# Kernel optimization log

Hardware: AMD Instinct MI355X
Metric: run time of the kernel (lower is better)

Reference implementation:

```python
import jax, jax.numpy as jnp
import numpy as np

B, T, D, H, F = 4, 2048, 1024, 16, 4096
HD = D // H
EPS = 1e-5


def setup_inputs() -> dict:
    key = jax.random.key(0)
    ks = jax.random.split(key, 10)
    s = lambda fan_in: 1.0 / np.sqrt(fan_in)
    return {
        "x": jax.random.normal(ks[0], (B, T, D), jnp.float32),
        "ln1_g": jnp.ones((D,), jnp.float32),
        "ln1_b": jnp.zeros((D,), jnp.float32),
        "ln2_g": jnp.ones((D,), jnp.float32),
        "ln2_b": jnp.zeros((D,), jnp.float32),
        "Wq": jax.random.normal(ks[1], (H, D, HD), jnp.float32) * s(D),
        "Wk": jax.random.normal(ks[2], (H, D, HD), jnp.float32) * s(D),
        "Wv": jax.random.normal(ks[3], (H, D, HD), jnp.float32) * s(D),
        "Wo": jax.random.normal(ks[4], (D, D), jnp.float32) * s(D),
        "bo": jnp.zeros((D,), jnp.float32),
        "W1": jax.random.normal(ks[5], (D, F), jnp.float32) * s(D),
        "b1": jnp.zeros((F,), jnp.float32),
        "W2": jax.random.normal(ks[6], (F, D), jnp.float32) * s(F),
        "b2": jnp.zeros((D,), jnp.float32),
    }


def _layernorm(x, g, b):
    mu = jnp.mean(x, axis=-1, keepdims=True)
    var = jnp.mean(jnp.square(x - mu), axis=-1, keepdims=True)
    return (x - mu) * jax.lax.rsqrt(var + EPS) * g + b


def reference(x, ln1_g, ln1_b, ln2_g, ln2_b, Wq, Wk, Wv, Wo, bo, W1, b1, W2, b2):
    Bc, Tc, Dc = x.shape
    xn = _layernorm(x, ln1_g, ln1_b)
    # per-head projections (source loops over heads; here batched over h)
    q = jnp.einsum('btd,hdk->bhtk', xn, Wq)
    k = jnp.einsum('btd,hdk->bhtk', xn, Wk)
    v = jnp.einsum('btd,hdk->bhtk', xn, Wv)
    scale = jnp.asarray(Dc, x.dtype) ** -0.5  # C**-0.5 with C = embedding_dim
    scores = jnp.einsum('bhtk,bhsk->bhts', q, k) * scale
    causal = jnp.tril(jnp.ones((Tc, Tc), bool))
    scores = jnp.where(causal, scores, -jnp.inf)
    attn = jax.nn.softmax(scores, axis=-1)
    out = jnp.einsum('bhts,bhsk->bhtk', attn, v)
    out = out.transpose(0, 2, 1, 3).reshape(Bc, Tc, Dc)  # concat heads
    attn_out = out @ Wo + bo
    h = attn_out + x  # residual 1
    hn = _layernorm(h, ln2_g, ln2_b)
    ff = jax.nn.relu(hn @ W1 + b1) @ W2 + b2
    return ff + h  # residual 2
```

## Files before the change

### kernel.cpp

```cpp
#include <hip/hip_runtime.h>
#include <hip/hip_bf16.h>

#define NB 4
#define NT 2048
#define ND 1024
#define NH 16
#define NHD 64
#define NF 4096
#define MTOK (NB*NT)

typedef float f32x4 __attribute__((ext_vector_type(4)));
typedef __bf16 bf16x8 __attribute__((ext_vector_type(8)));
typedef short s16x8 __attribute__((ext_vector_type(8)));
typedef unsigned short ushort_t;

__device__ inline ushort_t f2bf(float f) {
    unsigned int u = __builtin_bit_cast(unsigned int, f);
    unsigned int r = (u + 0x7FFFu + ((u >> 16) & 1u)) >> 16;
    return (ushort_t)r;
}
__device__ inline float bf2f(ushort_t u) {
    return __builtin_bit_cast(float, (unsigned int)u << 16);
}

__device__ __forceinline__ void async_load16(const void* g, void* l) {
    __builtin_amdgcn_global_load_lds(
        (const __attribute__((address_space(1))) void*)g,
        (__attribute__((address_space(3))) void*)l, 16, 0, 0);
}

__device__ __forceinline__ unsigned int cvt_pk_bf16(float lo, float hi) {
    unsigned int r;
    asm("v_cvt_pk_bf16_f32 %0, %1, %2" : "=v"(r) : "v"(lo), "v"(hi));
    return r;
}

__device__ __forceinline__ float exp2_fast(float x) {
    float r;
    asm("v_exp_f32 %0, %1" : "=v"(r) : "v"(x));
    return r;
}

__global__ __launch_bounds__(256)
void transpose_to_bf16(const float* __restrict__ src, ushort_t* __restrict__ dst,
                       int R, int C) {
    __shared__ float tile[32][33];
    int c0 = blockIdx.x * 32, r0 = blockIdx.y * 32;
    #pragma unroll
    for (int i = 0; i < 32; i += 8)
        tile[threadIdx.y + i][threadIdx.x] =
            src[(size_t)(r0 + threadIdx.y + i) * C + c0 + threadIdx.x];
    __syncthreads();
    #pragma unroll
    for (int i = 0; i < 32; i += 8)
        dst[(size_t)(c0 + threadIdx.y + i) * R + r0 + threadIdx.x] =
            f2bf(tile[threadIdx.x][threadIdx.y + i]);
}

__global__ __launch_bounds__(256)
void transpose_qkv_to_bf16(const float* __restrict__ Wq, const float* __restrict__ Wk,
                           const float* __restrict__ Wv, ushort_t* __restrict__ dst) {
    __shared__ float tile[32][33];
    int z = blockIdx.z;
    int w = z >> 4, h = z & 15;
    const float* src = (w == 0 ? Wq : (w == 1 ? Wk : Wv)) + (size_t)h * ND * NHD;
    const float sc = (w == 0) ? 0.03125f * 1.44269504f : 1.0f;
    ushort_t* out = dst + ((size_t)w * ND + h * NHD) * ND;
    int c0 = blockIdx.x * 32, r0 = blockIdx.y * 32;
    #pragma unroll
    for (int i = 0; i < 32; i += 8)
        tile[threadIdx.y + i][threadIdx.x] =
            src[(size_t)(r0 + threadIdx.y + i) * NHD + c0 + threadIdx.x];
    __syncthreads();
    #pragma unroll
    for (int i = 0; i < 32; i += 8)
        out[(size_t)(c0 + threadIdx.y + i) * ND + r0 + threadIdx.x] =
            f2bf(tile[threadIdx.x][threadIdx.y + i] * sc);
}

__global__ __launch_bounds__(256)
void layernorm_to_bf16(const float* __restrict__ x, const float* __restrict__ g,
                       const float* __restrict__ bvec, ushort_t* __restrict__ out) {
    int row = blockIdx.x;
    const float4* xr = (const float4*)(x + (size_t)row * ND);
    float4 v = xr[threadIdx.x];
    float s = v.x + v.y + v.z + v.w;
    float s2 = v.x * v.x + v.y * v.y + v.z * v.z + v.w * v.w;
    #pragma unroll
    for (int o = 32; o >= 1; o >>= 1) {
        s += __shfl_xor(s, o);
        s2 += __shfl_xor(s2, o);
    }
    __shared__ float red[8];
    int wave = threadIdx.x >> 6, lane = threadIdx.x & 63;
    if (lane == 0) { red[wave] = s; red[4 + wave] = s2; }
    __syncthreads();
    float ts = red[0] + red[1] + red[2] + red[3];
    float ts2 = red[4] + red[5] + red[6] + red[7];
    float mu = ts * (1.f / ND);
    float var = ts2 * (1.f / ND) - mu * mu;
    float rs = rsqrtf(var + 1e-5f);
    float4 gv = ((const float4*)g)[threadIdx.x];
    float4 bv = ((const float4*)bvec)[threadIdx.x];
    ushort4 o4;
    o4.x = f2bf((v.x - mu) * rs * gv.x + bv.x);
    o4.y = f2bf((v.y - mu) * rs * gv.y + bv.y);
    o4.z = f2bf((v.z - mu) * rs * gv.z + bv.z);
    o4.w = f2bf((v.w - mu) * rs * gv.w + bv.w);
    ((ushort4*)(out + (size_t)row * ND))[threadIdx.x] = o4;
}

__global__ __launch_bounds__(256)
void layernorm_bf16(const ushort_t* __restrict__ x, const float* __restrict__ g,
                    const float* __restrict__ bvec, ushort_t* __restrict__ out) {
    int row = blockIdx.x;
    ushort4 u4 = ((const ushort4*)(x + (size_t)row * ND))[threadIdx.x];
    float4 v;
    v.x = bf2f(u4.x); v.y = bf2f(u4.y); v.z = bf2f(u4.z); v.w = bf2f(u4.w);
    float s = v.x + v.y + v.z + v.w;
    float s2 = v.x * v.x + v.y * v.y + v.z * v.z + v.w * v.w;
    #pragma unroll
    for (int o = 32; o >= 1; o >>= 1) {
        s += __shfl_xor(s, o);
        s2 += __shfl_xor(s2, o);
    }
    __shared__ float red[8];
    int wave = threadIdx.x >> 6, lane = threadIdx.x & 63;
    if (lane == 0) { red[wave] = s; red[4 + wave] = s2; }
    __syncthreads();
    float ts = red[0] + red[1] + red[2] + red[3];
    float ts2 = red[4] + red[5] + red[6] + red[7];
    float mu = ts * (1.f / ND);
    float var = ts2 * (1.f / ND) - mu * mu;
    float rs = rsqrtf(var + 1e-5f);
    float4 gv = ((const float4*)g)[threadIdx.x];
    float4 bv = ((const float4*)bvec)[threadIdx.x];
    ushort4 o4;
    o4.x = f2bf((v.x - mu) * rs * gv.x + bv.x);
    o4.y = f2bf((v.y - mu) * rs * gv.y + bv.y);
    o4.z = f2bf((v.z - mu) * rs * gv.z + bv.z);
    o4.w = f2bf((v.w - mu) * rs * gv.w + bv.w);
    ((ushort4*)(out + (size_t)row * ND))[threadIdx.x] = o4;
}

template<int BN, bool HAS_BIAS, bool RELU, int RES_MODE, bool OUT_F32, int OUT_MODE = 0>
__global__ __launch_bounds__(512, 2)
void gemm8p(const ushort_t* __restrict__ A, const ushort_t* __restrict__ Bt,
            const float* __restrict__ bias, const void* __restrict__ res,
            void* __restrict__ outp, ushort_t* __restrict__ vTp,
            int M, int N, int K) {
    constexpr int NFR = BN / 64;
    __shared__ __align__(16) ushort_t As[2][256 * 64];
    __shared__ __align__(16) ushort_t Bs[2][BN * 64];
    const int t = threadIdx.x;
    const int wave = t >> 6, lane = t & 63;
    const int wm = wave >> 2, wn = wave & 3;
    const int g = lane >> 4, l16 = lane & 15;
    int wid = blockIdx.y * gridDim.x + blockIdx.x;
    const int cpx = (gridDim.x * gridDim.y) >> 3;
    wid = (wid & 7) * cpx + (wid >> 3);
    const int m0 = (wid / gridDim.x) * 256;
    const int n0 = (wid % gridDim.x) * BN;
    const int lrow8 = lane >> 3;
    const int srcCol = ((lane & 7) ^ lrow8) * 8;
    const ushort_t* Abase = A + (size_t)m0 * K + srcCol;
    const ushort_t* Bbase = Bt + (size_t)n0 * K + srcCol;
    const int NKT = K >> 6;

    f32x4 acc[8][NFR] = {};

    auto stageAhalf = [&](int kt, int h, int slot) {
        #pragma unroll
        for (int j = 2 * h; j < 2 * h + 2; j++) {
            const int rowbase = j * 64 + wave * 8;
            async_load16(Abase + (size_t)(rowbase + lrow8) * K + kt * 64,
                         &As[slot][rowbase * 64]);
        }
    };
    auto stageBhalf = [&](int kt, int h, int slot) {
        if constexpr (BN == 256) {
            #pragma unroll
            for (int j = 2 * h; j < 2 * h + 2; j++) {
                const int rowbase = j * 64 + wave * 8;
                async_load16(Bbase + (size_t)(rowbase + lrow8) * K + kt * 64,
                             &Bs[slot][rowbase * 64]);
            }
        } else {
            const int rowbase = h * 64 + wave * 8;
            async_load16(Bbase + (size_t)(rowbase + lrow8) * K + kt * 64,
                         &Bs[slot][rowbase * 64]);
        }
    };

    stageAhalf(0, 0, 0); stageAhalf(0, 1, 0);
    stageBhalf(0, 0, 0); stageBhalf(0, 1, 0);
    stageBhalf(1, 0, 1); stageBhalf(1, 1, 1);
    stageAhalf(1, 0, 1);
    if constexpr (BN == 256) asm volatile("s_waitcnt vmcnt(6)" ::: "memory");
    else                     asm volatile("s_waitcnt vmcnt(4)" ::: "memory");
    __builtin_amdgcn_s_barrier();
    __builtin_amdgcn_sched_barrier(0);

    for (int kt = 0; kt < NKT; ++kt) {
        const int cur = kt & 1, nxt = cur ^ 1;
        const ushort_t* as = As[cur];
        const ushort_t* bs = Bs[cur];
        bf16x8 bfr[NFR][2];

        if constexpr (BN == 128) {
            #pragma unroll
            for (int ph = 0; ph < 2; ph++) {
                if (ph == 0) {
                    #pragma unroll
                    for (int nf = 0; nf < NFR; nf++)
                        #pragma unroll
                        for (int ks = 0; ks < 2; ks++) {
                            const int row = wn * (BN / 4) + nf * 16 + l16;
                            int a = row * 128 + ks * 64 + 16 * g;
                            a ^= (row & 7) << 4;
                            bfr[nf][ks] = *(const bf16x8*)((const char*)bs + a);
                        }
                }
                bf16x8 af[2][2][2];
                #pragma unroll
                for (int qq = 0; qq < 2; qq++)
                    #pragma unroll
                    for (int mi2 = 0; mi2 < 2; mi2++)
                        #pragma unroll
                        for (int ks = 0; ks < 2; ks++) {
                            const int row = (ph * 2 + qq) * 64 + wm * 32 + mi2 * 16 + l16;
                            int a = row * 128 + ks * 64 + 16 * g;
                            a ^= (row & 7) << 4;
                            af[qq][mi2][ks] = *(const bf16x8*)((const char*)as + a);
                        }
                if (ph == 0) {
                    if (kt + 1 < NKT) stageAhalf(kt + 1, 1, nxt);
                } else {
                    if (kt + 2 < NKT) {
                        stageBhalf(kt + 2, 0, cur);
                        stageBhalf(kt + 2, 1, cur);
                        stageAhalf(kt + 2, 0, cur);
                    }
                }
                __builtin_amdgcn_sched_barrier(0);
                if (ph == 1) {
                    if (kt >= NKT - 2) asm volatile("s_waitcnt vmcnt(0)" ::: "memory");
                    else               asm volatile("s_waitcnt vmcnt(4)" ::: "memory");
                }
                __builtin_amdgcn_s_barrier();
                __builtin_amdgcn_sched_barrier(0);
                __builtin_amdgcn_s_setprio(1);
                #pragma unroll
                for (int qq = 0; qq < 2; qq++)
                    #pragma unroll
                    for (int mi2 = 0; mi2 < 2; mi2++)
                        #pragma unroll
                        for (int nf = 0; nf < NFR; nf++)
                            #pragma unroll
                            for (int ks = 0; ks < 2; ks++)
                                acc[(ph * 2 + qq) * 2 + mi2][nf] =
                                    __builtin_amdgcn_mfma_f32_16x16x32_bf16(
                                        af[qq][mi2][ks], bfr[nf][ks],
                                        acc[(ph * 2 + qq) * 2 + mi2][nf], 0, 0, 0);
                __builtin_amdgcn_s_setprio(0);
                __builtin_amdgcn_s_barrier();
                __builtin_amdgcn_sched_barrier(0);
            }
        } else {
            #pragma unroll
            for (int q = 0; q < 4; q++) {
                if (q == 0) {
                    #pragma unroll
                    for (int nf = 0; nf < NFR; nf++)
                        #pragma unroll
                        for (int ks = 0; ks < 2; ks++) {
                            const int row = wn * (BN / 4) + nf * 16 + l16;
                            int a = row * 128 + ks * 64 + 16 * g;
                            a ^= (row & 7) << 4;
                            bfr[nf][ks] = *(const bf16x8*)((const char*)bs + a);
                        }
                }
                bf16x8 af[2][2];
                #pragma unroll
                for (int mi2 = 0; mi2 < 2; mi2++)
                    #pragma unroll
                    for (int ks = 0; ks < 2; ks++) {
                        const int row = q * 64 + wm * 32 + mi2 * 16 + l16;
                        int a = row * 128 + ks * 64 + 16 * g;
                        a ^= (row & 7) << 4;
                        af[mi2][ks] = *(const bf16x8*)((const char*)as + a);
                    }
                if (q == 0)      { if (kt + 1 < NKT) stageAhalf(kt + 1, 1, nxt); }
                else if (q == 1) { if (kt + 2 < NKT) stageBhalf(kt + 2, 0, cur); }
                else if (q == 2) { if (kt + 2 < NKT) stageBhalf(kt + 2, 1, cur); }
                else             { if (kt + 2 < NKT) stageAhalf(kt + 2, 0, cur); }
                __builtin_amdgcn_sched_barrier(0);
                if (q == 3) {
                    if (kt >= NKT - 2) asm volatile("s_waitcnt vmcnt(0)" ::: "memory");
                    else               asm volatile("s_waitcnt vmcnt(6)" ::: "memory");
                }
                __builtin_amdgcn_s_barrier();
                __builtin_amdgcn_sched_barrier(0);
                __builtin_amdgcn_s_setprio(1);
                #pragma unroll
                for (int mi2 = 0; mi2 < 2; mi2++)
                    #pragma unroll
                    for (int nf = 0; nf < NFR; nf++)
                        #pragma unroll
                        for (int ks = 0; ks < 2; ks++)
                            acc[q * 2 + mi2][nf] = __builtin_amdgcn_mfma_f32_16x16x32_bf16(
                                af[mi2][ks], bfr[nf][ks], acc[q * 2 + mi2][nf], 0, 0, 0);
                __builtin_amdgcn_s_setprio(0);
                __builtin_amdgcn_s_barrier();
                __builtin_amdgcn_sched_barrier(0);
            }
        }
    }

    const int gc0 = n0 + wn * (BN / 4) + l16;
    if constexpr (OUT_MODE == 1) {
        if (n0 >= 2048) {
            #pragma unroll
            for (int mi = 0; mi < 8; mi++) {
                const int rowb = m0 + (mi >> 1) * 64 + wm * 32 + (mi & 1) * 16 + g * 4;
                const int b = rowb >> 11, tt = rowb & 2047;
                #pragma unroll
                for (int nf = 0; nf < NFR; nf++) {
                    const int col = gc0 + nf * 16;
                    ushort4 o4;
                    o4.x = f2bf(acc[mi][nf][0]);
                    o4.y = f2bf(acc[mi][nf][1]);
                    o4.z = f2bf(acc[mi][nf][2]);
                    o4.w = f2bf(acc[mi][nf][3]);
                    *(ushort4*)(vTp + (size_t)(b * 1024 + col - 2048) * NT + tt) = o4;
                }
            }
            return;
        }
    }
    #pragma unroll
    for (int mi = 0; mi < 8; mi++) {
        const int rowb = m0 + (mi >> 1) * 64 + wm * 32 + (mi & 1) * 16 + g * 4;
        #pragma unroll
        for (int nf = 0; nf < NFR; nf++) {
            const int col = gc0 + nf * 16;
            float bb = 0.f;
            if constexpr (HAS_BIAS) bb = bias[col];
            #pragma unroll
            for (int r = 0; r < 4; r++) {
                const int row = rowb + r;
                float v = acc[mi][nf][r] + bb;
                if constexpr (RELU) v = fmaxf(v, 0.f);
                if constexpr (RES_MODE == 1)
                    v += ((const float*)res)[(size_t)row * N + col];
                else if constexpr (RES_MODE == 2)
                    v += bf2f(((const ushort_t*)res)[(size_t)row * N + col]);
                if constexpr (OUT_F32)
                    ((float*)outp)[(size_t)row * N + col] = v;
                else
                    ((ushort_t*)outp)[(size_t)row * N + col] = f2bf(v);
            }
        }
    }
}

template<bool HAS_BIAS, bool RELU, int RES_MODE, bool OUT_F32>
__global__ __launch_bounds__(256, 2)
void gemm2b64(const ushort_t* __restrict__ A, const ushort_t* __restrict__ Bt,
              const float* __restrict__ bias, const void* __restrict__ res,
              void* __restrict__ outp, int M, int N, int K) {
    __shared__ __align__(16) ushort_t As[2][128 * 64];
    __shared__ __align__(16) ushort_t Bs[2][128 * 64];
    const int t = threadIdx.x;
    const int wave = t >> 6, lane = t & 63;
    const int wm = wave >> 1, wn = wave & 1;
    const int g = lane >> 4, l16 = lane & 15;
    int wid = blockIdx.y * gridDim.x + blockIdx.x;
    const int cpx = (gridDim.x * gridDim.y) >> 3;
    wid = (wid & 7) * cpx + (wid >> 3);
    const int m0 = (wid / gridDim.x) * 128;
    const int n0 = (wid % gridDim.x) * 128;
    const int rw = lane >> 3, ck = lane & 7;
    const int srcCol = (ck ^ rw) * 8;
    const ushort_t* Abase = A + (size_t)m0 * K + srcCol;
    const ushort_t* Bbase = Bt + (size_t)n0 * K + srcCol;
    const int NKT = K >> 6;

    f32x4 acc[4][4] = {};

    auto stage = [&](int kt, int slot) {
        #pragma unroll
        for (int j = 0; j < 4; j++) {
            const int rowbase = j * 32 + wave * 8;
            async_load16(Abase + (size_t)(rowbase + rw) * K + kt * 64,
                         &As[slot][rowbase * 64]);
        }
        #pragma unroll
        for (int j = 0; j < 4; j++) {
            const int rowbase = j * 32 + wave * 8;
            async_load16(Bbase + (size_t)(rowbase + rw) * K + kt * 64,
                         &Bs[slot][rowbase * 64]);
        }
    };

    stage(0, 0);
    stage(1, 1);

    for (int kt = 0; kt < NKT; ++kt) {
        const int cur = kt & 1;
        if (kt >= NKT - 1) asm volatile("s_waitcnt vmcnt(0)" ::: "memory");
        else               asm volatile("s_waitcnt vmcnt(8)" ::: "memory");
        __builtin_amdgcn_s_barrier();
        __builtin_amdgcn_sched_barrier(0);

        const ushort_t* as = As[cur];
        const ushort_t* bs = Bs[cur];
        bf16x8 af[4][2], bfr[4][2];
        #pragma unroll
        for (int mi = 0; mi < 4; mi++)
            #pragma unroll
            for (int ks = 0; ks < 2; ks++) {
                const int row = wm * 64 + mi * 16 + l16;
                int a = row * 128 + ks * 64 + 16 * g;
                a ^= (row & 7) << 4;
                af[mi][ks] = *(const bf16x8*)((const char*)as + a);
            }
        #pragma unroll
        for (int nf = 0; nf < 4; nf++)
            #pragma unroll
            for (int ks = 0; ks < 2; ks++) {
                const int row = wn * 64 + nf * 16 + l16;
                int a = row * 128 + ks * 64 + 16 * g;
                a ^= (row & 7) << 4;
                bfr[nf][ks] = *(const bf16x8*)((const char*)bs + a);
            }
        __builtin_amdgcn_s_setprio(1);
        #pragma unroll
        for (int mi = 0; mi < 4; mi++)
            #pragma unroll
            for (int nf = 0; nf < 4; nf++)
                #pragma unroll
                for (int ks = 0; ks < 2; ks++)
                    acc[mi][nf] = __builtin_amdgcn_mfma_f32_16x16x32_bf16(
                        af[mi][ks], bfr[nf][ks], acc[mi][nf], 0, 0, 0);
        __builtin_amdgcn_s_setprio(0);
        __builtin_amdgcn_s_barrier();
        __builtin_amdgcn_sched_barrier(0);
        if (kt + 2 < NKT) stage(kt + 2, cur);
    }

    const int gc0 = n0 + wn * 64 + l16;
    #pragma unroll
    for (int mi = 0; mi < 4; mi++) {
        const int rowb = m0 + wm * 64 + mi * 16 + g * 4;
        #pragma unroll
        for (int nf = 0; nf < 4; nf++) {
            const int col = gc0 + nf * 16;
            float bb = 0.f;
            if constexpr (HAS_BIAS) bb = bias[col];
            #pragma unroll
            for (int r = 0; r < 4; r++) {
                const int row = rowb + r;
                float v = acc[mi][nf][r] + bb;
                if constexpr (RELU) v = fmaxf(v, 0.f);
                if constexpr (RES_MODE == 1)
                    v += ((const float*)res)[(size_t)row * N + col];
                else if constexpr (RES_MODE == 2)
                    v += bf2f(((const ushort_t*)res)[(size_t)row * N + col]);
                if constexpr (OUT_F32)
                    ((float*)outp)[(size_t)row * N + col] = v;
                else
                    ((ushort_t*)outp)[(size_t)row * N + col] = f2bf(v);
            }
        }
    }
}

__global__ __launch_bounds__(256)
void attn_kernel(const ushort_t* __restrict__ qkv, const ushort_t* __restrict__ vT,
                 ushort_t* __restrict__ out) {
    __shared__ __align__(16) ushort_t Ks[2][64 * 64];
    __shared__ __align__(16) ushort_t Vt[2][64 * 64];
    __shared__ unsigned int Pw[4][32][35];
    const int L = blockIdx.y * gridDim.x + blockIdx.x;
    const int xcd = L & 7, kk = L >> 3;
    const int bh = ((kk & 7) << 3) | xcd;
    const int pairIdx = kk >> 3;
    const int b = bh >> 4, h = bh & 15;
    const int t = threadIdx.x, wave = t >> 6, lane = t & 63;
    const int g = lane >> 4, q16 = lane & 15;
    const size_t base = ((size_t)b * NT) * 3072 + h * NHD;
    const ushort_t* qp_base = qkv + base;
    const ushort_t* kb = qkv + base + 1024;
    const ushort_t* vbt = vT + (size_t)bh * 64 * NT;
    const int krw = lane >> 3, kck = lane & 7;
    const int ksrc = (kck ^ krw) * 8;

    bf16x8 ones_f;
    {
        uint4 u = {0x3F803F80u, 0x3F803F80u, 0x3F803F80u, 0x3F803F80u};
        ones_f = __builtin_bit_cast(bf16x8, u);
    }

    auto stageK = [&](int kv, int buf) {
        #pragma unroll
        for (int c = 0; c < 2; c++) {
            const int rowbase = c * 32 + wave * 8;
            async_load16(kb + (size_t)(kv * 64 + rowbase + krw) * 3072 + ksrc,
                         &Ks[buf][rowbase * 64]);
        }
    };
    auto stageV = [&](int kv, int buf) {
        #pragma unroll
        for (int c = 0; c < 2; c++) {
            const int rowbase = c * 32 + wave * 8;
            const int scol = ((kck ^ krw ^ ((c * 4 + wave) & 7)) * 8);
            async_load16(vbt + (size_t)(rowbase + krw) * NT + kv * 64 + scol,
                         &Vt[buf][rowbase * 64]);
        }
    };

    for (int half = 0; half < 2; half++) {
        const int qt = half ? (15 - pairIdx) : pairIdx;
        const int q0 = qt * 128;
        const int wq0 = q0 + wave * 32;
        bf16x8 qf[2][2];
        #pragma unroll
        for (int qb2 = 0; qb2 < 2; qb2++) {
            const ushort_t* qp = qp_base + (size_t)(wq0 + 16 * qb2 + q16) * 3072 + 8 * g;
            qf[qb2][0] = *(const bf16x8*)qp;
            qf[qb2][1] = *(const bf16x8*)(qp + 32);
        }
        f32x4 of[2][4] = {};
        f32x4 of4[2] = {};
        const int nkv = 2 * qt + 2;

        stageK(0, 0);
        stageV(0, 0);
        __syncthreads();

        for (int kv = 0; kv < nkv; ++kv) {
            const int cur = kv & 1, nxt = cur ^ 1;
            if (kv + 1 < nkv) {
                stageK(kv + 1, nxt);
                stageV(kv + 1, nxt);
            }
            __builtin_amdgcn_sched_barrier(0);

            const int kbase = kv * 64;
            if (kbase <= wq0 + 31) {
                bf16x8 kf[4][2];
                #pragma unroll
                for (int n = 0; n < 4; n++)
                    #pragma unroll
                    for (int kd = 0; kd < 2; kd++) {
                        int row = n * 16 + q16;
                        int a = row * 128 + (kd * 64 + 16 * g);
                        a ^= ((row & 7) << 4);
                        kf[n][kd] = *(const bf16x8*)((const char*)&Ks[cur][0] + a);
                    }

                f32x4 sf[2][4] = {};
                #pragma unroll
                for (int n = 0; n < 4; n++)
                    #pragma unroll
                    for (int kd = 0; kd < 2; kd++) {
                        sf[0][n] = __builtin_amdgcn_mfma_f32_16x16x32_bf16(
                            kf[n][kd], qf[0][kd], sf[0][n], 0, 0, 0);
                        sf[1][n] = __builtin_amdgcn_mfma_f32_16x16x32_bf16(
                            kf[n][kd], qf[1][kd], sf[1][n], 0, 0, 0);
                    }

                #pragma unroll
                for (int qb2 = 0; qb2 < 2; qb2++) {
                    const int wqb = wq0 + 16 * qb2 + q16;
                    const bool partial = (kbase + 63 > wq0 + 16 * qb2);
                    float p[4][4];
                    #pragma unroll
                    for (int n = 0; n < 4; n++)
                        #pragma unroll
                        for (int r = 0; r < 4; r++) {
                            float v = sf[qb2][n][r];
                            if (partial) {
                                int kg = kbase + n * 16 + 4 * g + r;
                                if (kg > wqb) v = -1.0e30f;
                            }
                            p[n][r] = exp2_fast(v);
                        }
                    unsigned int* pr = &Pw[wave][16 * qb2 + q16][0];
                    #pragma unroll
                    for (int n = 0; n < 4; n++) {
                        pr[8 * n + 2 * g + 0] = cvt_pk_bf16(p[n][0], p[n][1]);
                        pr[8 * n + 2 * g + 1] = cvt_pk_bf16(p[n][2], p[n][3]);
                    }
                }

                #pragma unroll
                for (int kbk = 0; kbk < 2; kbk++) {
                    bf16x8 pfr[2];
                    #pragma unroll
                    for (int qb2 = 0; qb2 < 2; qb2++) {
                        const unsigned int* pr = &Pw[wave][16 * qb2 + q16][0];
                        uint4 pu;
                        pu.x = pr[16 * kbk + 4 * g + 0];
                        pu.y = pr[16 * kbk + 4 * g + 1];
                        pu.z = pr[16 * kbk + 4 * g + 2];
                        pu.w = pr[16 * kbk + 4 * g + 3];
                        pfr[qb2] = __builtin_bit_cast(bf16x8, pu);
                    }
                    of4[0] = __builtin_amdgcn_mfma_f32_16x16x32_bf16(
                        ones_f, pfr[0], of4[0], 0, 0, 0);
                    of4[1] = __builtin_amdgcn_mfma_f32_16x16x32_bf16(
                        ones_f, pfr[1], of4[1], 0, 0, 0);
                    #pragma unroll
                    for (int nf = 0; nf < 4; nf++) {
                        const int d = nf * 16 + q16;
                        int a = (d << 7) + (kbk * 64 + 16 * g);
                        a ^= (((d & 7) ^ ((d >> 3) & 7)) << 4);
                        bf16x8 vf = *(const bf16x8*)((const char*)&Vt[cur][0] + a);
                        of[0][nf] = __builtin_amdgcn_mfma_f32_16x16x32_bf16(
                            vf, pfr[0], of[0][nf], 0, 0, 0);
                        of[1][nf] = __builtin_amdgcn_mfma_f32_16x16x32_bf16(
                            vf, pfr[1], of[1][nf], 0, 0, 0);
                    }
                }
            }

            __syncthreads();
        }

        #pragma unroll
        for (int qb2 = 0; qb2 < 2; qb2++) {
            float rl = 1.f / of4[qb2][0];
            const size_t orow = (size_t)b * NT + q0 + wave * 32 + 16 * qb2 + q16;
            #pragma unroll
            for (int nf = 0; nf < 4; nf++) {
                ushort4 o4;
                o4.x = f2bf(of[qb2][nf][0] * rl);
                o4.y = f2bf(of[qb2][nf][1] * rl);
                o4.z = f2bf(of[qb2][nf][2] * rl);
                o4.w = f2bf(of[qb2][nf][3] * rl);
                *(ushort4*)(out + orow * ND + h * NHD + nf * 16 + 4 * g) = o4;
            }
        }
    }
}

extern "C" void kernel_launch(void* const* d_in, const int* in_sizes, int n_in,
                              void* d_out, int out_size, void* d_ws, size_t ws_size,
                              hipStream_t stream) {
    const float* x     = (const float*)d_in[0];
    const float* ln1_g = (const float*)d_in[1];
    const float* ln1_b = (const float*)d_in[2];
    const float* ln2_g = (const float*)d_in[3];
    const float* ln2_b = (const float*)d_in[4];
    const float* Wq    = (const float*)d_in[5];
    const float* Wk    = (const float*)d_in[6];
    const float* Wv    = (const float*)d_in[7];
    const float* Wo    = (const float*)d_in[8];
    const float* bo    = (const float*)d_in[9];
    const float* W1    = (const float*)d_in[10];
    const float* b1    = (const float*)d_in[11];
    const float* W2    = (const float*)d_in[12];
    const float* b2    = (const float*)d_in[13];
    float* outp = (float*)d_out;

    char* w = (char*)d_ws;
    ushort_t* Wqkv_t = (ushort_t*)(w);
    ushort_t* Wo_t   = (ushort_t*)(w + 6291456);
    ushort_t* W1_t   = (ushort_t*)(w + 8388608);
    ushort_t* W2_t   = (ushort_t*)(w + 16777216);
    ushort_t* xn     = (ushort_t*)(w + 25165824);
    ushort_t* qkv    = (ushort_t*)(w + 41943040);
    ushort_t* attn_o = qkv + (size_t)MTOK * 3072;
    ushort_t* ff1    = qkv;
    ushort_t* hbuf   = (ushort_t*)(w + 41943040 + 67108864);
    ushort_t* vT     = (ushort_t*)(w + 41943040 + 67108864 + 16777216);

    dim3 tb(32, 8);
    transpose_qkv_to_bf16<<<dim3(2, 32, 48), tb, 0, stream>>>(Wq, Wk, Wv, Wqkv_t);
    transpose_to_bf16<<<dim3(32, 32), tb, 0, stream>>>(Wo, Wo_t, 1024, 1024);
    transpose_to_bf16<<<dim3(128, 32), tb, 0, stream>>>(W1, W1_t, 1024, 4096);
    transpose_to_bf16<<<dim3(32, 128), tb, 0, stream>>>(W2, W2_t, 4096, 1024);

    layernorm_to_bf16<<<MTOK, 256, 0, stream>>>(x, ln1_g, ln1_b, xn);

    gemm8p<128, false, false, 0, false, 1><<<dim3(24, 32), 512, 0, stream>>>(
        xn, Wqkv_t, nullptr, nullptr, qkv, vT, MTOK, 3072, 1024);

    attn_kernel<<<dim3(8, 64), 256, 0, stream>>>(qkv, vT, attn_o);

    gemm8p<128, true, false, 1, false><<<dim3(8, 32), 512, 0, stream>>>(
        attn_o, Wo_t, bo, x, hbuf, nullptr, MTOK, 1024, 1024);

    layernorm_bf16<<<MTOK, 256, 0, stream>>>(hbuf, ln2_g, ln2_b, xn);

    gemm8p<256, true, true, 0, false><<<dim3(16, 32), 512, 0, stream>>>(
        xn, W1_t, b1, nullptr, ff1, nullptr, MTOK, NF, 1024);

    gemm2b64<true, false, 2, true><<<dim3(8, 64), 256, 0, stream>>>(
        ff1, W2_t, b2, hbuf, outp, MTOK, 1024, NF);
}
```

Before: 353.7 us.

## Move QKV and Wo GEMMs to 128x128 kernel, vectorize attention P LDS accesses

The QKV projection and output projection GEMMs now use the 128x128-tile gemm2b64 kernel (256 threads) instead of the 256x128 gemm8p variant, and the V-transpose epilogue moves into gemm2b64. gemm8p is specialized to BN=256 only, for the W1 GEMM. The attention kernel's P scratch row stride is padded from 35 to 36 words and aligned so P can be written as uint2 and read as uint4 vector LDS accesses instead of scalar ones. Smaller tiles give more blocks for these GEMMs but less data reuse per block, and the new padding may change LDS bank-conflict behavior.

```diff
diff --git a/kernel.cpp b/kernel.cpp
--- a/kernel.cpp
+++ b/kernel.cpp
@@ -143,12 +143,12 @@
     ((ushort4*)(out + (size_t)row * ND))[threadIdx.x] = o4;
 }
 
-template<int BN, bool HAS_BIAS, bool RELU, int RES_MODE, bool OUT_F32, int OUT_MODE = 0>
+template<bool HAS_BIAS, bool RELU, int RES_MODE, bool OUT_F32>
 __global__ __launch_bounds__(512, 2)
 void gemm8p(const ushort_t* __restrict__ A, const ushort_t* __restrict__ Bt,
             const float* __restrict__ bias, const void* __restrict__ res,
-            void* __restrict__ outp, ushort_t* __restrict__ vTp,
-            int M, int N, int K) {
+            void* __restrict__ outp, int M, int N, int K) {
+    constexpr int BN = 256;
     constexpr int NFR = BN / 64;
     __shared__ __align__(16) ushort_t As[2][256 * 64];
     __shared__ __align__(16) ushort_t Bs[2][BN * 64];
@@ -178,15 +178,9 @@
         }
     };
     auto stageBhalf = [&](int kt, int h, int slot) {
-        if constexpr (BN == 256) {
-            #pragma unroll
-            for (int j = 2 * h; j < 2 * h + 2; j++) {
-                const int rowbase = j * 64 + wave * 8;
-                async_load16(Bbase + (size_t)(rowbase + lrow8) * K + kt * 64,
-                             &Bs[slot][rowbase * 64]);
-            }
-        } else {
-            const int rowbase = h * 64 + wave * 8;
+        #pragma unroll
+        for (int j = 2 * h; j < 2 * h + 2; j++) {
+            const int rowbase = j * 64 + wave * 8;
             async_load16(Bbase + (size_t)(rowbase + lrow8) * K + kt * 64,
                          &Bs[slot][rowbase * 64]);
         }
@@ -196,8 +190,7 @@
     stageBhalf(0, 0, 0); stageBhalf(0, 1, 0);
     stageBhalf(1, 0, 1); stageBhalf(1, 1, 1);
     stageAhalf(1, 0, 1);
-    if constexpr (BN == 256) asm volatile("s_waitcnt vmcnt(6)" ::: "memory");
-    else                     asm volatile("s_waitcnt vmcnt(4)" ::: "memory");
+    asm volatile("s_waitcnt vmcnt(6)" ::: "memory");
     __builtin_amdgcn_s_barrier();
     __builtin_amdgcn_sched_barrier(0);
 
@@ -206,138 +199,56 @@
         const ushort_t* as = As[cur];
         const ushort_t* bs = Bs[cur];
         bf16x8 bfr[NFR][2];
-
-        if constexpr (BN == 128) {
-            #pragma unroll
-            for (int ph = 0; ph < 2; ph++) {
-                if (ph == 0) {
-                    #pragma unroll
-                    for (int nf = 0; nf < NFR; nf++)
-                        #pragma unroll
-                        for (int ks = 0; ks < 2; ks++) {
-                            const int row = wn * (BN / 4) + nf * 16 + l16;
-                            int a = row * 128 + ks * 64 + 16 * g;
-                            a ^= (row & 7) << 4;
-                            bfr[nf][ks] = *(const bf16x8*)((const char*)bs + a);
-                        }
-                }
-                bf16x8 af[2][2][2];
-                #pragma unroll
-                for (int qq = 0; qq < 2; qq++)
-                    #pragma unroll
-                    for (int mi2 = 0; mi2 < 2; mi2++)
-                        #pragma unroll
-                        for (int ks = 0; ks < 2; ks++) {
-                            const int row = (ph * 2 + qq) * 64 + wm * 32 + mi2 * 16 + l16;
-                            int a = row * 128 + ks * 64 + 16 * g;
-                            a ^= (row & 7) << 4;
-                            af[qq][mi2][ks] = *(const bf16x8*)((const char*)as + a);
-                        }
-                if (ph == 0) {
-                    if (kt + 1 < NKT) stageAhalf(kt + 1, 1, nxt);
-                } else {
-                    if (kt + 2 < NKT) {
-                        stageBhalf(kt + 2, 0, cur);
-                        stageBhalf(kt + 2, 1, cur);
-                        stageAhalf(kt + 2, 0, cur);
-                    }
-                }
-                __builtin_amdgcn_sched_barrier(0);
-                if (ph == 1) {
-                    if (kt >= NKT - 2) asm volatile("s_waitcnt vmcnt(0)" ::: "memory");
-                    else               asm volatile("s_waitcnt vmcnt(4)" ::: "memory");
-                }
-                __builtin_amdgcn_s_barrier();
-                __builtin_amdgcn_sched_barrier(0);
-                __builtin_amdgcn_s_setprio(1);
-                #pragma unroll
-                for (int qq = 0; qq < 2; qq++)
-                    #pragma unroll
-                    for (int mi2 = 0; mi2 < 2; mi2++)
-                        #pragma unroll
-                        for (int nf = 0; nf < NFR; nf++)
-                            #pragma unroll
-                            for (int ks = 0; ks < 2; ks++)
-                                acc[(ph * 2 + qq) * 2 + mi2][nf] =
-                                    __builtin_amdgcn_mfma_f32_16x16x32_bf16(
-                                        af[qq][mi2][ks], bfr[nf][ks],
-                                        acc[(ph * 2 + qq) * 2 + mi2][nf], 0, 0, 0);
-                __builtin_amdgcn_s_setprio(0);
-                __builtin_amdgcn_s_barrier();
-                __builtin_amdgcn_sched_barrier(0);
-            }
-        } else {
-            #pragma unroll
-            for (int q = 0; q < 4; q++) {
-                if (q == 0) {
-                    #pragma unroll
-                    for (int nf = 0; nf < NFR; nf++)
-                        #pragma unroll
-                        for (int ks = 0; ks < 2; ks++) {
-                            const int row = wn * (BN / 4) + nf * 16 + l16;
-                            int a = row * 128 + ks * 64 + 16 * g;
-                            a ^= (row & 7) << 4;
-                            bfr[nf][ks] = *(const bf16x8*)((const char*)bs + a);
-                        }
-                }
-                bf16x8 af[2][2];
-                #pragma unroll
-                for (int mi2 = 0; mi2 < 2; mi2++)
+        #pragma unroll
+        for (int q = 0; q < 4; q++) {
+            if (q == 0) {
+                #pragma unroll
+                for (int nf = 0; nf < NFR; nf++)
                     #pragma unroll
                     for (int ks = 0; ks < 2; ks++) {
-                        const int row = q * 64 + wm * 32 + mi2 * 16 + l16;
+                        const int row = wn * (BN / 4) + nf * 16 + l16;
                         int a = row * 128 + ks * 64 + 16 * g;
                         a ^= (row & 7) << 4;
-                        af[mi2][ks] = *(const bf16x8*)((const char*)as + a);
+                        bfr[nf][ks] = *(const bf16x8*)((const char*)bs + a);
                     }
-                if (q == 0)      { if (kt + 1 < NKT) stageAhalf(kt + 1, 1, nxt); }
-                else if (q == 1) { if (kt + 2 < NKT) stageBhalf(kt + 2, 0, cur); }
-                else if (q == 2) { if (kt + 2 < NKT) stageBhalf(kt + 2, 1, cur); }
-                else             { if (kt + 2 < NKT) stageAhalf(kt + 2, 0, cur); }
-                __builtin_amdgcn_sched_barrier(0);
-                if (q == 3) {
-                    if (kt >= NKT - 2) asm volatile("s_waitcnt vmcnt(0)" ::: "memory");
-                    else               asm volatile("s_waitcnt vmcnt(6)" ::: "memory");
+            }
+            bf16x8 af[2][2];
+            #pragma unroll
+            for (int mi2 = 0; mi2 < 2; mi2++)
+                #pragma unroll
+                for (int ks = 0; ks < 2; ks++) {
+                    const int row = q * 64 + wm * 32 + mi2 * 16 + l16;
+                    int a = row * 128 + ks * 64 + 16 * g;
+                    a ^= (row & 7) << 4;
+                    af[mi2][ks] = *(const bf16x8*)((const char*)as + a);
                 }
-                __builtin_amdgcn_s_barrier();
-                __builtin_amdgcn_sched_barrier(0);
-                __builtin_amdgcn_s_setprio(1);
-                #pragma unroll
-                for (int mi2 = 0; mi2 < 2; mi2++)
-                    #pragma unroll
-                    for (int nf = 0; nf < NFR; nf++)
-                        #pragma unroll
-                        for (int ks = 0; ks < 2; ks++)
-                            acc[q * 2 + mi2][nf] = __builtin_amdgcn_mfma_f32_16x16x32_bf16(
-                                af[mi2][ks], bfr[nf][ks], acc[q * 2 + mi2][nf], 0, 0, 0);
-                __builtin_amdgcn_s_setprio(0);
-                __builtin_amdgcn_s_barrier();
-                __builtin_amdgcn_sched_barrier(0);
-            }
+            if (q == 0)      { if (kt + 1 < NKT) stageAhalf(kt + 1, 1, nxt); }
+            else if (q == 1) { if (kt + 2 < NKT) stageBhalf(kt + 2, 0, cur); }
+            else if (q == 2) { if (kt + 2 < NKT) stageBhalf(kt + 2, 1, cur); }
+            else             { if (kt + 2 < NKT) stageAhalf(kt + 2, 0, cur); }
+            __builtin_amdgcn_sched_barrier(0);
+            if (q == 3) {
+                if (kt >= NKT - 2) asm volatile("s_waitcnt vmcnt(0)" ::: "memory");
+                else               asm volatile("s_waitcnt vmcnt(6)" ::: "memory");
+            }
+            __builtin_amdgcn_s_barrier();
+            __builtin_amdgcn_sched_barrier(0);
+            __builtin_amdgcn_s_setprio(1);
+            #pragma unroll
+            for (int mi2 = 0; mi2 < 2; mi2++)
+                #pragma unroll
+                for (int nf = 0; nf < NFR; nf++)
+                    #pragma unroll
+                    for (int ks = 0; ks < 2; ks++)
+                        acc[q * 2 + mi2][nf] = __builtin_amdgcn_mfma_f32_16x16x32_bf16(
+                            af[mi2][ks], bfr[nf][ks], acc[q * 2 + mi2][nf], 0, 0, 0);
+            __builtin_amdgcn_s_setprio(0);
+            __builtin_amdgcn_s_barrier();
+            __builtin_amdgcn_sched_barrier(0);
         }
     }
 
     const int gc0 = n0 + wn * (BN / 4) + l16;
-    if constexpr (OUT_MODE == 1) {
-        if (n0 >= 2048) {
-            #pragma unroll
-            for (int mi = 0; mi < 8; mi++) {
-                const int rowb = m0 + (mi >> 1) * 64 + wm * 32 + (mi & 1) * 16 + g * 4;
-                const int b = rowb >> 11, tt = rowb & 2047;
-                #pragma unroll
-                for (int nf = 0; nf < NFR; nf++) {
-                    const int col = gc0 + nf * 16;
-                    ushort4 o4;
-                    o4.x = f2bf(acc[mi][nf][0]);
-                    o4.y = f2bf(acc[mi][nf][1]);
-                    o4.z = f2bf(acc[mi][nf][2]);
-                    o4.w = f2bf(acc[mi][nf][3]);
-                    *(ushort4*)(vTp + (size_t)(b * 1024 + col - 2048) * NT + tt) = o4;
-                }
-            }
-            return;
-        }
-    }
     #pragma unroll
     for (int mi = 0; mi < 8; mi++) {
         const int rowb = m0 + (mi >> 1) * 64 + wm * 32 + (mi & 1) * 16 + g * 4;
@@ -364,11 +275,12 @@
     }
 }
 
-template<bool HAS_BIAS, bool RELU, int RES_MODE, bool OUT_F32>
+template<bool HAS_BIAS, bool RELU, int RES_MODE, bool OUT_F32, int OUT_MODE = 0>
 __global__ __launch_bounds__(256, 2)
 void gemm2b64(const ushort_t* __restrict__ A, const ushort_t* __restrict__ Bt,
               const float* __restrict__ bias, const void* __restrict__ res,
-              void* __restrict__ outp, int M, int N, int K) {
+              void* __restrict__ outp, ushort_t* __restrict__ vTp,
+              int M, int N, int K) {
     __shared__ __align__(16) ushort_t As[2][128 * 64];
     __shared__ __align__(16) ushort_t Bs[2][128 * 64];
     const int t = threadIdx.x;
@@ -450,6 +362,26 @@
     }
 
     const int gc0 = n0 + wn * 64 + l16;
+    if constexpr (OUT_MODE == 1) {
+        if (n0 >= 2048) {
+            #pragma unroll
+            for (int mi = 0; mi < 4; mi++) {
+                const int rowb = m0 + wm * 64 + mi * 16 + g * 4;
+                const int b = rowb >> 11, tt = rowb & 2047;
+                #pragma unroll
+                for (int nf = 0; nf < 4; nf++) {
+                    const int col = gc0 + nf * 16;
+                    ushort4 o4;
+                    o4.x = f2bf(acc[mi][nf][0]);
+                    o4.y = f2bf(acc[mi][nf][1]);
+                    o4.z = f2bf(acc[mi][nf][2]);
+                    o4.w = f2bf(acc[mi][nf][3]);
+                    *(ushort4*)(vTp + (size_t)(b * 1024 + col - 2048) * NT + tt) = o4;
+                }
+            }
+            return;
+        }
+    }
     #pragma unroll
     for (int mi = 0; mi < 4; mi++) {
         const int rowb = m0 + wm * 64 + mi * 16 + g * 4;
@@ -481,7 +413,7 @@
                  ushort_t* __restrict__ out) {
     __shared__ __align__(16) ushort_t Ks[2][64 * 64];
     __shared__ __align__(16) ushort_t Vt[2][64 * 64];
-    __shared__ unsigned int Pw[4][32][35];
+    __shared__ __align__(16) unsigned int Pw[4][32][36];
     const int L = blockIdx.y * gridDim.x + blockIdx.x;
     const int xcd = L & 7, kk = L >> 3;
     const int bh = ((kk & 7) << 3) | xcd;
@@ -590,8 +522,10 @@
                     unsigned int* pr = &Pw[wave][16 * qb2 + q16][0];
                     #pragma unroll
                     for (int n = 0; n < 4; n++) {
-                        pr[8 * n + 2 * g + 0] = cvt_pk_bf16(p[n][0], p[n][1]);
-                        pr[8 * n + 2 * g + 1] = cvt_pk_bf16(p[n][2], p[n][3]);
+                        uint2 wv;
+                        wv.x = cvt_pk_bf16(p[n][0], p[n][1]);
+                        wv.y = cvt_pk_bf16(p[n][2], p[n][3]);
+                        *(uint2*)(pr + 8 * n + 2 * g) = wv;
                     }
                 }
 
@@ -601,11 +535,7 @@
                     #pragma unroll
                     for (int qb2 = 0; qb2 < 2; qb2++) {
                         const unsigned int* pr = &Pw[wave][16 * qb2 + q16][0];
-                        uint4 pu;
-                        pu.x = pr[16 * kbk + 4 * g + 0];
-                        pu.y = pr[16 * kbk + 4 * g + 1];
-                        pu.z = pr[16 * kbk + 4 * g + 2];
-                        pu.w = pr[16 * kbk + 4 * g + 3];
+                        uint4 pu = *(const uint4*)(pr + 16 * kbk + 4 * g);
                         pfr[qb2] = __builtin_bit_cast(bf16x8, pu);
                     }
                     of4[0] = __builtin_amdgcn_mfma_f32_16x16x32_bf16(
@@ -685,19 +615,19 @@
 
     layernorm_to_bf16<<<MTOK, 256, 0, stream>>>(x, ln1_g, ln1_b, xn);
 
-    gemm8p<128, false, false, 0, false, 1><<<dim3(24, 32), 512, 0, stream>>>(
+    gemm2b64<false, false, 0, false, 1><<<dim3(24, 64), 256, 0, stream>>>(
         xn, Wqkv_t, nullptr, nullptr, qkv, vT, MTOK, 3072, 1024);
 
     attn_kernel<<<dim3(8, 64), 256, 0, stream>>>(qkv, vT, attn_o);
 
-    gemm8p<128, true, false, 1, false><<<dim3(8, 32), 512, 0, stream>>>(
+    gemm2b64<true, false, 1, false><<<dim3(8, 64), 256, 0, stream>>>(
         attn_o, Wo_t, bo, x, hbuf, nullptr, MTOK, 1024, 1024);
 
     layernorm_bf16<<<MTOK, 256, 0, stream>>>(hbuf, ln2_g, ln2_b, xn);
 
-    gemm8p<256, true, true, 0, false><<<dim3(16, 32), 512, 0, stream>>>(
-        xn, W1_t, b1, nullptr, ff1, nullptr, MTOK, NF, 1024);
+    gemm8p<true, true, 0, false><<<dim3(16, 32), 512, 0, stream>>>(
+        xn, W1_t, b1, nullptr, ff1, MTOK, NF, 1024);
 
     gemm2b64<true, false, 2, true><<<dim3(8, 64), 256, 0, stream>>>(
-        ff1, W2_t, b2, hbuf, outp, MTOK, 1024, NF);
-}
+        ff1, W2_t, b2, hbuf, outp, nullptr, MTOK, 1024, NF);
+}
```

Result: faster. 344.6 us, median of 3 (-2.6%).
